# Kernel optimization log

Measured on AMD Instinct MI355X. Metric: run time of the kernel, lower is better.

## Reference

```python
import jax, jax.numpy as jnp
import numpy as np

N = 1048576   # total nodes across the mini-batch
D = 128       # node feature dim
B = 2048      # number of graphs (segments)


def setup_inputs() -> dict:
    key = jax.random.key(0)
    x = jax.random.normal(key, (N, D), dtype=jnp.float32)
    # sorted segment ids, every segment 0..B-1 non-empty (~512 nodes each)
    batch = ((jnp.arange(N, dtype=jnp.int64) * B) // N).astype(jnp.int32)
    return {"x": x, "batch": batch, "num_segments": B}


def reference(x, batch, num_segments):
    # Faithful to: for bi in range(batch.max()+1): out.append(x[batch==bi].max(0)[0])
    # expressed as a single-pass segment max (indices are sorted).
    return jax.ops.segment_max(x, batch, num_segments=num_segments,
                               indices_are_sorted=True)
```

## Files before the change

kernel.cpp:

```cpp
#include <hip/hip_runtime.h>
#include <math.h>


__global__ __launch_bounds__(256) void find_bounds_kernel(
    const int* __restrict__ batch, int* __restrict__ bounds, int N, int B) {
    int b = blockIdx.x * 256 + threadIdx.x;
    if (b > B) return;
    if (b == B) { bounds[B] = N; return; }
    int lo = 0, hi = N;
    while (lo < hi) {
        int mid = (lo + hi) >> 1;
        if (batch[mid] < b) lo = mid + 1; else hi = mid;
    }
    bounds[b] = lo;
}

__device__ __forceinline__ float4 max4(float4 a, float4 b) {
    a.x = fmaxf(a.x, b.x);
    a.y = fmaxf(a.y, b.y);
    a.z = fmaxf(a.z, b.z);
    a.w = fmaxf(a.w, b.w);
    return a;
}

__global__ __launch_bounds__(256, 8) void seg_max_kernel(
    const float* __restrict__ x, const int* __restrict__ bounds,
    float* __restrict__ out) {
    const int seg   = blockIdx.x;
    const int start = bounds[seg];
    const int end   = bounds[seg + 1];

    const int tid  = threadIdx.x;
    const int col4 = tid & 31;
    const int rg   = tid >> 5;

    const float4* __restrict__ x4 = reinterpret_cast<const float4*>(x);
    const float4 ninf = make_float4(-INFINITY, -INFINITY, -INFINITY, -INFINITY);
    float4 m0 = ninf, m1 = ninf, m2 = ninf, m3 = ninf;

    int r = start + rg;
    for (; r + 24 < end; r += 32) {
        float4 v0 = x4[(size_t)(r)      * 32 + col4];
        float4 v1 = x4[(size_t)(r + 8)  * 32 + col4];
        float4 v2 = x4[(size_t)(r + 16) * 32 + col4];
        float4 v3 = x4[(size_t)(r + 24) * 32 + col4];
        m0 = max4(m0, v0);
        m1 = max4(m1, v1);
        m2 = max4(m2, v2);
        m3 = max4(m3, v3);
    }
    for (; r < end; r += 8) {
        m0 = max4(m0, x4[(size_t)r * 32 + col4]);
    }
    float4 m = max4(max4(m0, m1), max4(m2, m3));

    __shared__ float4 smem[256];
    smem[tid] = m;
    __syncthreads();
    #pragma unroll
    for (int step = 128; step >= 32; step >>= 1) {
        if (tid < step) {
            smem[tid] = max4(smem[tid], smem[tid + step]);
        }
        __syncthreads();
    }
    if (tid < 32) {
        reinterpret_cast<float4*>(out)[(size_t)seg * 32 + tid] = smem[tid];
    }
}

extern "C" void kernel_launch(void* const* d_in, const int* in_sizes, int n_in,
                              void* d_out, int out_size, void* d_ws, size_t ws_size,
                              hipStream_t stream) {
    const float* x     = (const float*)d_in[0];
    const int*   batch = (const int*)d_in[1];
    float*       out   = (float*)d_out;
    int*         bounds = (int*)d_ws;

    const int D = 128;
    const int N = in_sizes[0] / D;
    const int B = out_size / D;

    find_bounds_kernel<<<(B + 1 + 255) / 256, 256, 0, stream>>>(batch, bounds, N, B);
    seg_max_kernel<<<B, 256, 0, stream>>>(x, bounds, out);
}
```

Baseline: 105.3 us.

## Replace binary-search bounds with boundary scan and give each row group a contiguous range

The bounds kernel now streams the batch array once and writes segment starts wherever adjacent ids differ, replacing per-segment binary searches that make many dependent global loads. In the max kernel each of the eight row groups now reduces its own contiguous block of rows instead of interleaved rows, using pointer increments with a 4-way unrolled loop. The scan launches far more threads to read the 4 MB id array, which costs bandwidth in exchange for removing serial search latency. Contiguous per-group ranges change the access pattern, which may help or hurt DRAM locality.

```diff
diff --git a/kernel.cpp b/kernel.cpp
--- a/kernel.cpp
+++ b/kernel.cpp
@@ -2,17 +2,34 @@
 #include <math.h>
 
 
-__global__ __launch_bounds__(256) void find_bounds_kernel(
+__global__ __launch_bounds__(256) void bounds_scan_kernel(
     const int* __restrict__ batch, int* __restrict__ bounds, int N, int B) {
-    int b = blockIdx.x * 256 + threadIdx.x;
-    if (b > B) return;
-    if (b == B) { bounds[B] = N; return; }
-    int lo = 0, hi = N;
-    while (lo < hi) {
-        int mid = (lo + hi) >> 1;
-        if (batch[mid] < b) lo = mid + 1; else hi = mid;
+    int g  = blockIdx.x * 256 + threadIdx.x;
+    int i0 = g * 4;
+    if (i0 >= N) return;
+
+    int v[5];
+    if (i0 + 3 < N) {
+        int4 c = reinterpret_cast<const int4*>(batch)[g];
+        v[0] = c.x; v[1] = c.y; v[2] = c.z; v[3] = c.w;
+    } else {
+        for (int j = 0; j < 4; ++j) v[j] = (i0 + j < N) ? batch[i0 + j] : 0;
     }
-    bounds[b] = lo;
+    v[4] = (i0 + 4 < N) ? batch[i0 + 4] : 0;
+
+    if (g == 0) {
+        for (int s = 0; s <= v[0]; ++s) bounds[s] = 0;
+    }
+    #pragma unroll
+    for (int j = 0; j < 4; ++j) {
+        int i = i0 + j;
+        if (i + 1 < N) {
+            if (v[j] != v[j + 1])
+                for (int s = v[j] + 1; s <= v[j + 1]; ++s) bounds[s] = i + 1;
+        } else {
+            for (int s = v[j] + 1; s <= B; ++s) bounds[s] = N;
+        }
+    }
 }
 
 __device__ __forceinline__ float4 max4(float4 a, float4 b) {
@@ -34,24 +51,29 @@
     const int col4 = tid & 31;
     const int rg   = tid >> 5;
 
+    const int len = end - start;
+    const int cb  = len >> 3;
+    const int rem = len & 7;
+    const int gs  = start + rg * cb + (rg < rem ? rg : rem);
+    const int ge  = gs + cb + (rg < rem ? 1 : 0);
+
     const float4* __restrict__ x4 = reinterpret_cast<const float4*>(x);
     const float4 ninf = make_float4(-INFINITY, -INFINITY, -INFINITY, -INFINITY);
     float4 m0 = ninf, m1 = ninf, m2 = ninf, m3 = ninf;
 
-    int r = start + rg;
-    for (; r + 24 < end; r += 32) {
-        float4 v0 = x4[(size_t)(r)      * 32 + col4];
-        float4 v1 = x4[(size_t)(r + 8)  * 32 + col4];
-        float4 v2 = x4[(size_t)(r + 16) * 32 + col4];
-        float4 v3 = x4[(size_t)(r + 24) * 32 + col4];
+    const float4* __restrict__ p = x4 + (size_t)gs * 32 + col4;
+    int r = gs;
+    for (; r + 3 < ge; r += 4, p += 128) {
+        float4 v0 = p[0];
+        float4 v1 = p[32];
+        float4 v2 = p[64];
+        float4 v3 = p[96];
         m0 = max4(m0, v0);
         m1 = max4(m1, v1);
         m2 = max4(m2, v2);
         m3 = max4(m3, v3);
     }
-    for (; r < end; r += 8) {
-        m0 = max4(m0, x4[(size_t)r * 32 + col4]);
-    }
+    for (; r < ge; ++r, p += 32) m0 = max4(m0, p[0]);
     float4 m = max4(max4(m0, m1), max4(m2, m3));
 
     __shared__ float4 smem[256];
@@ -72,15 +94,16 @@
 extern "C" void kernel_launch(void* const* d_in, const int* in_sizes, int n_in,
                               void* d_out, int out_size, void* d_ws, size_t ws_size,
                               hipStream_t stream) {
-    const float* x     = (const float*)d_in[0];
-    const int*   batch = (const int*)d_in[1];
-    float*       out   = (float*)d_out;
+    const float* x      = (const float*)d_in[0];
+    const int*   batch  = (const int*)d_in[1];
+    float*       out    = (float*)d_out;
     int*         bounds = (int*)d_ws;
 
     const int D = 128;
     const int N = in_sizes[0] / D;
     const int B = out_size / D;
 
-    find_bounds_kernel<<<(B + 1 + 255) / 256, 256, 0, stream>>>(batch, bounds, N, B);
+    const int chunks = (N + 3) / 4;
+    bounds_scan_kernel<<<(chunks + 255) / 256, 256, 0, stream>>>(batch, bounds, N, B);
     seg_max_kernel<<<B, 256, 0, stream>>>(x, bounds, out);
 }
```

New measurement: 107.1 us. No clear change (+1.8%).

## Partition rows evenly across blocks with atomic max merging at segment edges

Applied to the files above, without the earlier changes.

Replaces the per-segment grid (which needed a separate bounds-search kernel) with a fixed row-chunked grid. Each block finds segment boundaries inside its chunk with local binary searches and reduces each piece. Partial segments that cross a chunk edge merge through integer atomic max/min tricks; interior segments write directly. Loads switch to nontemporal, and an init kernel fills the output with -inf. The intent is balanced work for skewed segment sizes, at the cost of an extra launch, atomics and more per-block control flow.

```diff
diff --git a/kernel.cpp b/kernel.cpp
--- a/kernel.cpp
+++ b/kernel.cpp
@@ -2,20 +2,9 @@
 #include <math.h>
 
 
-__global__ __launch_bounds__(256) void find_bounds_kernel(
-    const int* __restrict__ batch, int* __restrict__ bounds, int N, int B) {
-    int b = blockIdx.x * 256 + threadIdx.x;
-    if (b > B) return;
-    if (b == B) { bounds[B] = N; return; }
-    int lo = 0, hi = N;
-    while (lo < hi) {
-        int mid = (lo + hi) >> 1;
-        if (batch[mid] < b) lo = mid + 1; else hi = mid;
-    }
-    bounds[b] = lo;
-}
+typedef float f32x4 __attribute__((ext_vector_type(4)));
 
-__device__ __forceinline__ float4 max4(float4 a, float4 b) {
+__device__ __forceinline__ f32x4 max4(f32x4 a, f32x4 b) {
     a.x = fmaxf(a.x, b.x);
     a.y = fmaxf(a.y, b.y);
     a.z = fmaxf(a.z, b.z);
@@ -23,49 +12,101 @@
     return a;
 }
 
-__global__ __launch_bounds__(256, 8) void seg_max_kernel(
-    const float* __restrict__ x, const int* __restrict__ bounds,
-    float* __restrict__ out) {
-    const int seg   = blockIdx.x;
-    const int start = bounds[seg];
-    const int end   = bounds[seg + 1];
+__device__ __forceinline__ void atomic_max_f32(float* addr, float v) {
+    if (v >= 0.0f) atomicMax((int*)addr, __float_as_int(v));
+    else           atomicMin((unsigned int*)addr, __float_as_uint(v));
+}
+
+__global__ __launch_bounds__(256) void init_out_kernel(float4* out4, int n4) {
+    int i = blockIdx.x * 256 + threadIdx.x;
+    if (i < n4)
+        out4[i] = make_float4(-INFINITY, -INFINITY, -INFINITY, -INFINITY);
+}
+
+__global__ __launch_bounds__(256, 4) void seg_max_rows_kernel(
+    const float* __restrict__ x, const int* __restrict__ batch,
+    float* __restrict__ out, int N, int R) {
+    const int r0 = blockIdx.x * R;
+    if (r0 >= N) return;
+    const int r1 = min(r0 + R, N);
 
     const int tid  = threadIdx.x;
     const int col4 = tid & 31;
     const int rg   = tid >> 5;
 
-    const float4* __restrict__ x4 = reinterpret_cast<const float4*>(x);
-    const float4 ninf = make_float4(-INFINITY, -INFINITY, -INFINITY, -INFINITY);
-    float4 m0 = ninf, m1 = ninf, m2 = ninf, m3 = ninf;
+    const int sFirst = batch[r0];
+    const int sLast  = batch[r1 - 1];
 
-    int r = start + rg;
-    for (; r + 24 < end; r += 32) {
-        float4 v0 = x4[(size_t)(r)      * 32 + col4];
-        float4 v1 = x4[(size_t)(r + 8)  * 32 + col4];
-        float4 v2 = x4[(size_t)(r + 16) * 32 + col4];
-        float4 v3 = x4[(size_t)(r + 24) * 32 + col4];
-        m0 = max4(m0, v0);
-        m1 = max4(m1, v1);
-        m2 = max4(m2, v2);
-        m3 = max4(m3, v3);
-    }
-    for (; r < end; r += 8) {
-        m0 = max4(m0, x4[(size_t)r * 32 + col4]);
-    }
-    float4 m = max4(max4(m0, m1), max4(m2, m3));
+    const f32x4* __restrict__ x4 = reinterpret_cast<const f32x4*>(x);
+    __shared__ f32x4 smem[256];
 
-    __shared__ float4 smem[256];
-    smem[tid] = m;
-    __syncthreads();
-    #pragma unroll
-    for (int step = 128; step >= 32; step >>= 1) {
-        if (tid < step) {
-            smem[tid] = max4(smem[tid], smem[tid + step]);
+    for (int s = sFirst; s <= sLast; ++s) {
+        int a = r0, b = r1;
+        if (s > sFirst) {
+            int lo = r0, hi = r1;
+            while (lo < hi) {
+                int mid = (lo + hi) >> 1;
+                if (batch[mid] < s) lo = mid + 1; else hi = mid;
+            }
+            a = lo;
+        }
+        if (s < sLast) {
+            int lo = a, hi = r1;
+            while (lo < hi) {
+                int mid = (lo + hi) >> 1;
+                if (batch[mid] <= s) lo = mid + 1; else hi = mid;
+            }
+            b = lo;
+        }
+        if (a < b) {
+            const int len = b - a;
+            const int cb  = len >> 3;
+            const int rem = len & 7;
+            const int gs  = a + rg * cb + (rg < rem ? rg : rem);
+            const int ge  = gs + cb + (rg < rem ? 1 : 0);
+
+            f32x4 m0 = {-INFINITY, -INFINITY, -INFINITY, -INFINITY};
+            f32x4 m1 = m0, m2 = m0, m3 = m0;
+
+            const f32x4* p = x4 + (size_t)gs * 32 + col4;
+            int r = gs;
+            for (; r + 3 < ge; r += 4, p += 128) {
+                f32x4 v0 = __builtin_nontemporal_load(p);
+                f32x4 v1 = __builtin_nontemporal_load(p + 32);
+                f32x4 v2 = __builtin_nontemporal_load(p + 64);
+                f32x4 v3 = __builtin_nontemporal_load(p + 96);
+                m0 = max4(m0, v0);
+                m1 = max4(m1, v1);
+                m2 = max4(m2, v2);
+                m3 = max4(m3, v3);
+            }
+            for (; r < ge; ++r, p += 32) m0 = max4(m0, __builtin_nontemporal_load(p));
+            f32x4 m = max4(max4(m0, m1), max4(m2, m3));
+
+            smem[tid] = m;
+            __syncthreads();
+            #pragma unroll
+            for (int step = 128; step >= 32; step >>= 1) {
+                if (tid < step) smem[tid] = max4(smem[tid], smem[tid + step]);
+                __syncthreads();
+            }
+
+            if (tid < 32) {
+                f32x4 v = smem[tid];
+                const bool edge = (a == r0 && r0 > 0 && batch[r0 - 1] == s) ||
+                                  (b == r1 && r1 < N && batch[r1] == s);
+                float* o = out + (size_t)s * 128 + col4 * 4;
+                if (edge) {
+                    atomic_max_f32(o + 0, v.x);
+                    atomic_max_f32(o + 1, v.y);
+                    atomic_max_f32(o + 2, v.z);
+                    atomic_max_f32(o + 3, v.w);
+                } else {
+                    *reinterpret_cast<float4*>(o) = make_float4(v.x, v.y, v.z, v.w);
+                }
+            }
         }
         __syncthreads();
-    }
-    if (tid < 32) {
-        reinterpret_cast<float4*>(out)[(size_t)seg * 32 + tid] = smem[tid];
     }
 }
 
@@ -75,12 +116,14 @@
     const float* x     = (const float*)d_in[0];
     const int*   batch = (const int*)d_in[1];
     float*       out   = (float*)d_out;
-    int*         bounds = (int*)d_ws;
 
     const int D = 128;
     const int N = in_sizes[0] / D;
-    const int B = out_size / D;
 
-    find_bounds_kernel<<<(B + 1 + 255) / 256, 256, 0, stream>>>(batch, bounds, N, B);
-    seg_max_kernel<<<B, 256, 0, stream>>>(x, bounds, out);
+    const int n4 = out_size / 4;
+    init_out_kernel<<<(n4 + 255) / 256, 256, 0, stream>>>((float4*)d_out, n4);
+
+    const int R    = (N + 2047) / 2048;
+    const int grid = (N + R - 1) / R;
+    seg_max_rows_kernel<<<grid, 256, 0, stream>>>(x, batch, out, N, R);
 }
```

Result: faster. 100.3 us (median of 2 runs) (-4.7%).
